# Performance work log

Measured on AMD Instinct MI355X. Metric: run time of the kernel, lower is better.

Reference implementation:

```python
import jax, jax.numpy as jnp
import numpy as np

B, T, P = 32, 400, 10000  # batch, num_tf, num_peak


def setup_inputs() -> dict:
    key = jax.random.key(0)
    k_x, k_w, k_fc = jax.random.split(key, 3)
    x = jax.random.normal(k_x, (B, T, P), dtype=jnp.float32)
    W = jax.random.normal(k_w, (T, P), dtype=jnp.float32)
    fc1_w = jax.random.normal(k_fc, (1, T * P), dtype=jnp.float32) * 0.01
    fc1_b = jnp.zeros((1,), dtype=jnp.float32)
    return {"x": x, "W": W, "fc1_w": fc1_w, "fc1_b": fc1_b}


def reference(x, W, fc1_w, fc1_b):
    # x: [B, T, P]; W: [T, P]; fc1_w: [1, T*P]; fc1_b: [1]
    # out_b = sum_{t,p} x[b,t,p] * |W[t,p]| * fc1_w[0, t*P+p] + fc1_b
    xw = x * jnp.abs(W)[None, :, :]            # [B, T, P]
    flat = xw.reshape(x.shape[0], -1)          # [B, T*P]
    out = flat @ fc1_w.T + fc1_b               # [B, 1]
    return out
```

## Files before the change

### kernel.cpp

```cpp
#include <hip/hip_runtime.h>

#define BATCH 32
#define NELEM 4000000
#define N4 (NELEM / 4)
#define BLK 256
#define NBLK 512
#define CHUNK ((N4 + NBLK - 1) / NBLK)
#define WPB (BLK / 64)
#define PSTRIDE (NBLK * WPB)

typedef float f4 __attribute__((ext_vector_type(4)));

__global__ __launch_bounds__(BLK)
void stage1_kernel(const f4* __restrict__ x,
                   const f4* __restrict__ W,
                   const f4* __restrict__ F,
                   float* __restrict__ partials) {
    __shared__ f4 s_lds[CHUNK];
    const int bx = blockIdx.x;
    const int t  = threadIdx.x;
    const int i0 = bx * CHUNK;
    const int len = (i0 + CHUNK <= N4) ? CHUNK : (N4 - i0);

    for (int i = t; i < len; i += BLK) {
        f4 wv = W[i0 + i];
        f4 fv = F[i0 + i];
        f4 s;
        s.x = fabsf(wv.x) * fv.x;
        s.y = fabsf(wv.y) * fv.y;
        s.z = fabsf(wv.z) * fv.z;
        s.w = fabsf(wv.w) * fv.w;
        s_lds[i] = s;
    }
    __syncthreads();

    const int lane = t & 63;
    const int wid  = t >> 6;

    for (int r = 0; r < BATCH; ++r) {
        const f4* __restrict__ xr = x + (size_t)r * N4 + i0;
        float acc[4] = {0.f, 0.f, 0.f, 0.f};
        #pragma unroll
        for (int k = 0; k < 8; ++k) {
            const int i = k * BLK + t;
            if (i < len) {
                f4 xv = __builtin_nontemporal_load(xr + i);
                f4 sv = s_lds[i];
                acc[k & 3] += xv.x * sv.x + xv.y * sv.y
                            + xv.z * sv.z + xv.w * sv.w;
            }
        }
        float a = (acc[0] + acc[1]) + (acc[2] + acc[3]);
        #pragma unroll
        for (int off = 32; off > 0; off >>= 1)
            a += __shfl_down(a, off, 64);
        if (lane == 0)
            partials[(size_t)r * PSTRIDE + bx * WPB + wid] = a;
    }
}

__global__ __launch_bounds__(64)
void stage2_kernel(const float* __restrict__ partials,
                   const float* __restrict__ fc1_b,
                   float* __restrict__ out) {
    const int b    = blockIdx.x;
    const int lane = threadIdx.x;
    float t = 0.0f;
    for (int k = lane; k < PSTRIDE; k += 64) t += partials[(size_t)b * PSTRIDE + k];
    #pragma unroll
    for (int off = 32; off > 0; off >>= 1) t += __shfl_down(t, off, 64);
    if (lane == 0) out[b] = t + fc1_b[0];
}

extern "C" void kernel_launch(void* const* d_in, const int* in_sizes, int n_in,
                              void* d_out, int out_size, void* d_ws, size_t ws_size,
                              hipStream_t stream) {
    const float* x     = (const float*)d_in[0];
    const float* W     = (const float*)d_in[1];
    const float* fc1_w = (const float*)d_in[2];
    const float* fc1_b = (const float*)d_in[3];
    float* out      = (float*)d_out;
    float* partials = (float*)d_ws;

    stage1_kernel<<<NBLK, BLK, 0, stream>>>(
        (const f4*)x, (const f4*)W, (const f4*)fc1_w, partials);
    stage2_kernel<<<BATCH, 64, 0, stream>>>(partials, fc1_b, out);
}
```

Measured before the change: 713.0 us.

## Split work over chunk×batch grid and recompute weights per block instead of LDS

Stage 1 now launches a 2D grid of 64 chunks by 32 batch rows. Each block streams its x slice and reloads W and fc1_w from global memory (served by L2/cache) rather than staging |W|*F in LDS and looping over all batch rows. This raises parallelism from 512 blocks to 2048 and removes the large LDS allocation that limited occupancy. The cost is re-reading W and F once per batch row, which puts more pressure on L2/MALL bandwidth. Stage 2 shrinks to a single load per lane since there are now 64 partials per row.

```diff
diff --git a/kernel.cpp b/kernel.cpp
--- a/kernel.cpp
+++ b/kernel.cpp
@@ -4,59 +4,56 @@
 #define NELEM 4000000
 #define N4 (NELEM / 4)
 #define BLK 256
-#define NBLK 512
-#define CHUNK ((N4 + NBLK - 1) / NBLK)
-#define WPB (BLK / 64)
-#define PSTRIDE (NBLK * WPB)
+#define CHUNKS 64
+#define CHUNK (N4 / CHUNKS)
 
 typedef float f4 __attribute__((ext_vector_type(4)));
+
+__device__ __forceinline__ float dot1(const f4* __restrict__ xr,
+                                      const f4* __restrict__ W,
+                                      const f4* __restrict__ F, int i) {
+    f4 wv = W[i];
+    f4 fv = F[i];
+    f4 xv = __builtin_nontemporal_load(xr + i);
+    return xv.x * fabsf(wv.x) * fv.x + xv.y * fabsf(wv.y) * fv.y
+         + xv.z * fabsf(wv.z) * fv.z + xv.w * fabsf(wv.w) * fv.w;
+}
 
 __global__ __launch_bounds__(BLK)
 void stage1_kernel(const f4* __restrict__ x,
                    const f4* __restrict__ W,
                    const f4* __restrict__ F,
                    float* __restrict__ partials) {
-    __shared__ f4 s_lds[CHUNK];
-    const int bx = blockIdx.x;
-    const int t  = threadIdx.x;
-    const int i0 = bx * CHUNK;
-    const int len = (i0 + CHUNK <= N4) ? CHUNK : (N4 - i0);
+    const int c = blockIdx.x;
+    const int r = blockIdx.y;
+    const int t = threadIdx.x;
+    const int i0 = c * CHUNK;
+    const int i1 = i0 + CHUNK;
+    const f4* __restrict__ xr = x + (size_t)r * N4;
 
-    for (int i = t; i < len; i += BLK) {
-        f4 wv = W[i0 + i];
-        f4 fv = F[i0 + i];
-        f4 s;
-        s.x = fabsf(wv.x) * fv.x;
-        s.y = fabsf(wv.y) * fv.y;
-        s.z = fabsf(wv.z) * fv.z;
-        s.w = fabsf(wv.w) * fv.w;
-        s_lds[i] = s;
+    float a0 = 0.f, a1 = 0.f, a2 = 0.f, a3 = 0.f;
+    int i = i0 + t;
+    for (; i + 3 * BLK < i1; i += 4 * BLK) {
+        a0 += dot1(xr, W, F, i);
+        a1 += dot1(xr, W, F, i + BLK);
+        a2 += dot1(xr, W, F, i + 2 * BLK);
+        a3 += dot1(xr, W, F, i + 3 * BLK);
     }
-    __syncthreads();
+    for (; i < i1; i += BLK)
+        a0 += dot1(xr, W, F, i);
 
+    float a = (a0 + a1) + (a2 + a3);
+    #pragma unroll
+    for (int off = 32; off > 0; off >>= 1)
+        a += __shfl_down(a, off, 64);
+
+    __shared__ float lds[BLK / 64];
     const int lane = t & 63;
     const int wid  = t >> 6;
-
-    for (int r = 0; r < BATCH; ++r) {
-        const f4* __restrict__ xr = x + (size_t)r * N4 + i0;
-        float acc[4] = {0.f, 0.f, 0.f, 0.f};
-        #pragma unroll
-        for (int k = 0; k < 8; ++k) {
-            const int i = k * BLK + t;
-            if (i < len) {
-                f4 xv = __builtin_nontemporal_load(xr + i);
-                f4 sv = s_lds[i];
-                acc[k & 3] += xv.x * sv.x + xv.y * sv.y
-                            + xv.z * sv.z + xv.w * sv.w;
-            }
-        }
-        float a = (acc[0] + acc[1]) + (acc[2] + acc[3]);
-        #pragma unroll
-        for (int off = 32; off > 0; off >>= 1)
-            a += __shfl_down(a, off, 64);
-        if (lane == 0)
-            partials[(size_t)r * PSTRIDE + bx * WPB + wid] = a;
-    }
+    if (lane == 0) lds[wid] = a;
+    __syncthreads();
+    if (t == 0)
+        partials[(size_t)r * CHUNKS + c] = lds[0] + lds[1] + lds[2] + lds[3];
 }
 
 __global__ __launch_bounds__(64)
@@ -65,8 +62,7 @@
                    float* __restrict__ out) {
     const int b    = blockIdx.x;
     const int lane = threadIdx.x;
-    float t = 0.0f;
-    for (int k = lane; k < PSTRIDE; k += 64) t += partials[(size_t)b * PSTRIDE + k];
+    float t = partials[(size_t)b * CHUNKS + lane];
     #pragma unroll
     for (int off = 32; off > 0; off >>= 1) t += __shfl_down(t, off, 64);
     if (lane == 0) out[b] = t + fc1_b[0];
@@ -82,7 +78,8 @@
     float* out      = (float*)d_out;
     float* partials = (float*)d_ws;
 
-    stage1_kernel<<<NBLK, BLK, 0, stream>>>(
+    dim3 grid(CHUNKS, BATCH);
+    stage1_kernel<<<grid, BLK, 0, stream>>>(
         (const f4*)x, (const f4*)W, (const f4*)fc1_w, partials);
     stage2_kernel<<<BATCH, 64, 0, stream>>>(partials, fc1_b, out);
 }
```

Measured after the change: 693.9 us. 1.03x faster.
